# Performance work log

Hardware: AMD Instinct MI355X
Metric: run time of the kernel (lower is better)

## Reference

```python
import jax, jax.numpy as jnp
import numpy as np
from jax import lax

B, C_IN, H, W = 32, 128, 64, 64
K, C_OUT, KS = 8, 128, 3
HID = C_IN * 4  # extend = 4
TEMPERATURE = 1.0
PAD = 1


def setup_inputs() -> dict:
    key = jax.random.key(0)
    ks = jax.random.split(key, 7)
    x = jax.random.normal(ks[0], (B, C_IN, H, W), jnp.float32)
    prompt_param = jax.random.uniform(ks[1], (1, K, HID), jnp.float32)
    w1 = jax.random.normal(ks[2], (HID, C_IN), jnp.float32) * 0.05
    b1 = jnp.zeros((HID,), jnp.float32)
    w2 = jax.random.normal(ks[3], (HID, HID), jnp.float32) * 0.05
    b2 = jnp.zeros((HID,), jnp.float32)
    kernels_weights = jax.random.normal(ks[4], (K, C_OUT, C_IN, KS, KS), jnp.float32) * 0.05
    kernels_bias = jax.random.normal(ks[5], (K, C_OUT), jnp.float32) * 0.05
    return {
        'x': x, 'prompt_param': prompt_param,
        'w1': w1, 'b1': b1, 'w2': w2, 'b2': b2,
        'kernels_weights': kernels_weights, 'kernels_bias': kernels_bias,
    }


def reference(x, prompt_param, w1, b1, w2, b2, kernels_weights, kernels_bias):
    # Attention: global avg pool -> MLP -> prompt dot -> softmax over kernels
    pooled = jnp.mean(x, axis=(2, 3))                       # (B, C_in)
    h = jax.nn.relu(pooled @ w1.T + b1)                     # (B, HID)
    s = h @ w2.T + b2                                       # (B, HID)
    scores = jnp.sum(s[:, None, :] * prompt_param, axis=-1)  # (B, K)
    alphas = jax.nn.softmax(scores / TEMPERATURE, axis=-1)   # (B, K)

    # Per-sample kernel aggregation
    agg_w = jnp.einsum('bk,koihw->boihw', alphas, kernels_weights)  # (B,O,I,kh,kw)
    agg_b = alphas @ kernels_bias                                    # (B, O)

    # Per-sample conv2d (equivalent to the groups=B grouped-conv trick)
    def conv_one(xi, wi):
        # xi: (C_in,H,W), wi: (O,C_in,kh,kw)
        return lax.conv_general_dilated(
            xi[None], wi, window_strides=(1, 1),
            padding=((PAD, PAD), (PAD, PAD)),
            dimension_numbers=('NCHW', 'OIHW', 'NCHW'))[0]
    out = jax.vmap(conv_one)(x, agg_w)                       # (B,O,H,W)
    out = out + agg_b[:, :, None, None]
    return out
```

## Files before the change

kernel.cpp:

```cpp
#include <hip/hip_runtime.h>
#include <hip/hip_bf16.h>
#include <stdint.h>


typedef __bf16 v8bf __attribute__((ext_vector_type(8)));
typedef float  v4f  __attribute__((ext_vector_type(4)));

#define XT_OFF     0u
#define XT_BYTES   (32u*4096u*128u*2u)
#define AGGW_OFF   (XT_OFF + XT_BYTES)
#define AGGW_BYTES (32u*9u*128u*128u*2u)
#define PART_OFF   (AGGW_OFF)
#define POOLED_OFF (AGGW_OFF + 0x100000u)
#define H_OFF      (AGGW_OFF + 0x110000u)
#define PSCORE_OFF (AGGW_OFF + 0x120000u)
#define ALPHA_OFF  (AGGW_OFF + AGGW_BYTES)
#define ALPHA_BYTES (32u*8u*4u)
#define AGGB_OFF   (ALPHA_OFF + ALPHA_BYTES)
#define AGGB_BYTES (32u*128u*4u)

typedef const void __attribute__((address_space(1))) gconst_t;
typedef void       __attribute__((address_space(3))) ldsv_t;

__device__ __forceinline__ void g2l16(const void* g, void* l) {
  __builtin_amdgcn_global_load_lds((gconst_t*)g, (ldsv_t*)l, 16, 0, 0);
}

__global__ __launch_bounds__(256) void pool_convert_kernel(
    const float* __restrict__ x, float* __restrict__ partial,
    __hip_bfloat16* __restrict__ xT) {
  const int b = blockIdx.x >> 6;
  const int h = blockIdx.x & 63;
  const int tid = threadIdx.x;
  const int wv = tid >> 6, lane = tid & 63;
  __shared__ __align__(16) __hip_bfloat16 sT[64 * 130];

  const float* xrow = x + (((size_t)b * 128) << 12) + (h << 6);
  for (int i = 0; i < 32; ++i) {
    int c = wv * 32 + i;
    float v = xrow[((size_t)c << 12) + lane];
    sT[lane * 130 + c] = __float2bfloat16(v);
    float s = v;
    #pragma unroll
    for (int m = 32; m > 0; m >>= 1) s += __shfl_xor(s, m);
    if (lane == 0) partial[((b << 6) + h) * 128 + c] = s;
  }
  __syncthreads();
  const int pw = tid >> 2;
  const int piece = tid & 3;
  const uint32_t* s32 = (const uint32_t*)sT;
  uint32_t vals[16];
  #pragma unroll
  for (int j = 0; j < 16; ++j) vals[j] = s32[pw * 65 + piece * 16 + j];
  char* dst = (char*)xT + ((((size_t)b << 6) + h) * 64 + pw) * 256 + piece * 64;
  #pragma unroll
  for (int j = 0; j < 4; ++j)
    ((uint4*)dst)[j] = make_uint4(vals[4*j], vals[4*j+1], vals[4*j+2], vals[4*j+3]);
}

__global__ __launch_bounds__(128) void pool_reduce_kernel(
    const float* __restrict__ partial, float* __restrict__ pooled) {
  const int b = blockIdx.x, c = threadIdx.x;
  float acc = 0.0f;
  const float* src = partial + ((size_t)b << 6) * 128 + c;
  #pragma unroll 8
  for (int h = 0; h < 64; ++h) acc += src[h * 128];
  pooled[b * 128 + c] = acc * (1.0f / 4096.0f);
}

__global__ __launch_bounds__(256) void attn_l1_kernel(
    const float* __restrict__ pooled, const float* __restrict__ w1,
    const float* __restrict__ b1, float* __restrict__ hbuf) {
  const int jt = blockIdx.x * 8;
  const int tid = threadIdx.x;
  __shared__ float sW[8 * 132];
  __shared__ float sPool[32 * 132];

  {
    int r = tid >> 5, c4 = (tid & 31) * 4;
    *(float4*)&sW[r * 132 + c4] = *(const float4*)&w1[(jt + r) * 128 + c4];
  }
  #pragma unroll
  for (int q = 0; q < 4; ++q) {
    int idx = q * 256 + tid;
    int bb = idx >> 5, c4 = (idx & 31) * 4;
    *(float4*)&sPool[bb * 132 + c4] = *(const float4*)&pooled[bb * 128 + c4];
  }
  __syncthreads();

  const int b = tid >> 3, jr = tid & 7;
  float acc = 0.0f;
  #pragma unroll
  for (int i4 = 0; i4 < 32; ++i4) {
    float4 pv = *(const float4*)&sPool[b * 132 + i4 * 4];
    float4 wv = *(const float4*)&sW[jr * 132 + i4 * 4];
    acc += pv.x * wv.x + pv.y * wv.y + pv.z * wv.z + pv.w * wv.w;
  }
  hbuf[b * 512 + jt + jr] = fmaxf(acc + b1[jt + jr], 0.0f);
}

__global__ __launch_bounds__(256) void attn_l2s_kernel(
    const float* __restrict__ hbuf, const float* __restrict__ w2,
    const float* __restrict__ b2, const float* __restrict__ prompt,
    float* __restrict__ pscore) {
  const int jtile = blockIdx.x >> 1;
  const int bg = blockIdx.x & 1;
  const int jt = jtile * 8;
  const int tid = threadIdx.x;
  __shared__ float sW2[8 * 516];
  __shared__ float sH[16 * 516];
  __shared__ float sSc[16 * 9];
  __shared__ float sPr[64];

  #pragma unroll
  for (int q = 0; q < 4; ++q) {
    int idx = q * 256 + tid;
    int r = idx >> 7, c4 = (idx & 127) * 4;
    *(float4*)&sW2[r * 516 + c4] = *(const float4*)&w2[(jt + r) * 512 + c4];
  }
  #pragma unroll
  for (int q = 0; q < 8; ++q) {
    int idx = q * 256 + tid;
    int r = idx >> 7, c4 = (idx & 127) * 4;
    *(float4*)&sH[r * 516 + c4] =
        *(const float4*)&hbuf[(bg * 16 + r) * 512 + c4];
  }
  if (tid < 64) sPr[tid] = prompt[(tid >> 3) * 512 + jt + (tid & 7)];
  __syncthreads();

  const int pair = tid >> 1, half = tid & 1;
  const int bl = pair >> 3, jr = pair & 7;
  float acc = 0.0f;
  #pragma unroll
  for (int i4 = 0; i4 < 64; ++i4) {
    int idx = (half * 64 + i4) * 4;
    float4 hv = *(const float4*)&sH[bl * 516 + idx];
    float4 wv = *(const float4*)&sW2[jr * 516 + idx];
    acc += hv.x * wv.x + hv.y * wv.y + hv.z * wv.z + hv.w * wv.w;
  }
  acc += __shfl_xor(acc, 1);
  if (half == 0) sSc[bl * 9 + jr] = acc + b2[jt + jr];
  __syncthreads();

  if (tid < 128) {
    int bl = tid >> 3, k = tid & 7;
    float p = 0.0f;
    #pragma unroll
    for (int jj = 0; jj < 8; ++jj) p = fmaf(sSc[bl * 9 + jj], sPr[k * 8 + jj], p);
    pscore[((size_t)(jtile * 32 + bg * 16 + bl)) * 8 + k] = p;
  }
}

__global__ __launch_bounds__(256) void softmax_aggb_kernel(
    const float* __restrict__ pscore, const float* __restrict__ kbias,
    float* __restrict__ alphas, float* __restrict__ aggb) {
  const int b = blockIdx.x;
  const int tid = threadIdx.x;
  __shared__ float sRed[32 * 8], sSc[8], sA[8];

  {
    int jt2 = tid >> 3, k = tid & 7;
    sRed[jt2 * 8 + k] = pscore[((size_t)(jt2 * 32 + b)) * 8 + k] +
                        pscore[((size_t)((jt2 + 32) * 32 + b)) * 8 + k];
  }
  __syncthreads();
  if (tid < 8) {
    float sc = 0.0f;
    #pragma unroll
    for (int j = 0; j < 32; ++j) sc += sRed[j * 8 + tid];
    sSc[tid] = sc;
  }
  __syncthreads();
  if (tid == 0) {
    float mx = sSc[0];
    for (int k = 1; k < 8; ++k) mx = fmaxf(mx, sSc[k]);
    float sum = 0.0f, e[8];
    for (int k = 0; k < 8; ++k) { e[k] = expf(sSc[k] - mx); sum += e[k]; }
    float inv = 1.0f / sum;
    for (int k = 0; k < 8; ++k) sA[k] = e[k] * inv;
  }
  __syncthreads();
  if (tid < 8) alphas[b * 8 + tid] = sA[tid];
  if (tid < 128) {
    float acc = 0.0f;
    #pragma unroll
    for (int k = 0; k < 8; ++k) acc = fmaf(sA[k], kbias[k * 128 + tid], acc);
    aggb[b * 128 + tid] = acc;
  }
}

__global__ __launch_bounds__(128) void agg_weights_kernel(
    const float* __restrict__ kw, const float* __restrict__ alphas,
    __hip_bfloat16* __restrict__ aggw) {
  const int co = blockIdx.x;
  const int bg = blockIdx.y;
  const int tid = threadIdx.x;
  __shared__ float sA[64];
  __shared__ float sbuf[1152];
  if (tid < 64) sA[tid] = alphas[bg * 64 + tid];
  __syncthreads();

  float acc[8][9];
  #pragma unroll
  for (int bb = 0; bb < 8; ++bb)
    #pragma unroll
    for (int q = 0; q < 9; ++q) acc[bb][q] = 0.0f;

  for (int k = 0; k < 8; ++k) {
    const float* src = kw + ((size_t)(k * 128 + co)) * 1152;
    float v[9];
    #pragma unroll
    for (int q = 0; q < 9; ++q) v[q] = src[tid + 128 * q];
    #pragma unroll
    for (int bb = 0; bb < 8; ++bb) {
      float a = sA[bb * 8 + k];
      #pragma unroll
      for (int q = 0; q < 9; ++q) acc[bb][q] = fmaf(a, v[q], acc[bb][q]);
    }
  }

  #pragma unroll 1
  for (int bb = 0; bb < 8; ++bb) {
    __syncthreads();
    #pragma unroll
    for (int q = 0; q < 9; ++q) sbuf[tid + 128 * q] = acc[bb][q];
    __syncthreads();
    const int b = bg * 8 + bb;
    #pragma unroll
    for (int t = 0; t < 9; ++t)
      aggw[(((size_t)(b * 9 + t) * 128 + co) << 7) + tid] =
          __float2bfloat16(sbuf[tid * 9 + t]);
  }
}

#define XTILE_B 33792
#define ATILE_B 8192

__global__ __launch_bounds__(256) void dyn_conv_kernel(
    const __hip_bfloat16* __restrict__ xT, const __hip_bfloat16* __restrict__ aggw,
    const float* __restrict__ aggb, float* __restrict__ out) {
  const int tile = blockIdx.x;
  const int b    = blockIdx.y;
  const int tid  = threadIdx.x;
  const int wv = tid >> 6, lane = tid & 63;
  const int wm = wv >> 1, wn = wv & 1;
  const int lm = lane & 15, quad = lane >> 4;
  const int r0 = tile * 2;

  __shared__ __align__(16) char smem[XTILE_B + 2 * ATILE_B + 512];
  char* xb = smem;
  char* abuf = smem + XTILE_B;
  float* sBias = (float*)(smem + XTILE_B + 2 * ATILE_B);

  if (tid < 128) sBias[tid] = aggb[b * 128 + tid];

  for (int pos = tid; pos < 264; pos += 256) {
    int tr = pos / 66, tc = pos - tr * 66;
    int h = r0 - 1 + tr, w = tc - 1;
    if ((unsigned)h >= 64u || (unsigned)w >= 64u) {
      int4* d = (int4*)(xb + pos * 128);
      #pragma unroll
      for (int i = 0; i < 8; ++i) d[i] = make_int4(0, 0, 0, 0);
    }
  }

  const char* xTb = (const char*)xT + ((size_t)b << 20);
  const char* awb = (const char*)aggw + (size_t)b * 294912;

  auto stageX = [&](int half) {
    for (int i = wv; i < 33; i += 4) {
      int P = (i << 6) + lane;
      int pos = P >> 3, slot = P & 7;
      int tr = pos / 66, tc = pos - tr * 66;
      int h = r0 - 1 + tr, w = tc - 1;
      char* dst = xb + (i << 10);
      if ((unsigned)h < 64u && (unsigned)w < 64u) {
        int p = slot ^ (pos & 7);
        const char* src = xTb + (((h << 6) + w) << 8) + (half << 7) + (p << 4);
        g2l16(src, dst);
      }
    }
  };
  auto stageA = [&](int c) {
    int tap = (c % 18) >> 1;
    int cic = ((c / 18) << 1) | (c & 1);
    char* ab = abuf + (c & 1) * ATILE_B;
    const char* base = awb + (tap << 15);
    #pragma unroll
    for (int jj = 0; jj < 2; ++jj) {
      int j = wv * 2 + jj;
      int co = (j << 4) + (lane >> 2);
      int f = lane & 3;
      int p = f ^ ((co >> 1) & 3);
      const char* src = base + (co << 8) + (cic << 6) + (p << 4);
      g2l16(src, ab + (j << 10));
    }
  };

  int posb[4];
  #pragma unroll
  for (int ni = 0; ni < 4; ++ni) {
    int n = wn * 64 + ni * 16 + lm;
    posb[ni] = (n >> 6) * 66 + (n & 63);
  }
  const int fA = (quad ^ ((lm >> 1) & 3)) << 4;
  int aoff[4];
  #pragma unroll
  for (int mi = 0; mi < 4; ++mi) {
    int co = wm * 64 + mi * 16 + lm;
    aoff[mi] = (co << 6) + fA;
  }

  v4f acc[4][4];
  #pragma unroll
  for (int mi = 0; mi < 4; ++mi)
    #pragma unroll
    for (int ni = 0; ni < 4; ++ni) acc[mi][ni] = v4f{0.f, 0.f, 0.f, 0.f};

  auto computeChunk = [&](int c) {
    int tap = (c % 18) >> 1, sub = c & 1;
    int th = tap / 3, tw = tap - th * 3;
    char* ab = abuf + (c & 1) * ATILE_B;
    v8bf af[4], bfr[4];
    #pragma unroll
    for (int mi = 0; mi < 4; ++mi) af[mi] = *(const v8bf*)(ab + aoff[mi]);
    const int piece = (sub << 2) | quad;
    #pragma unroll
    for (int ni = 0; ni < 4; ++ni) {
      int pos = posb[ni] + th * 66 + tw;
      int pp = (piece ^ (pos & 7)) << 4;
      bfr[ni] = *(const v8bf*)(xb + (pos << 7) + pp);
    }
    #pragma unroll
    for (int mi = 0; mi < 4; ++mi)
      #pragma unroll
      for (int ni = 0; ni < 4; ++ni)
        acc[mi][ni] = __builtin_amdgcn_mfma_f32_16x16x32_bf16(
            af[mi], bfr[ni], acc[mi][ni], 0, 0, 0);
  };

  stageX(0);
  stageA(0);
  __syncthreads();
  for (int c = 0; c < 18; ++c) {
    if (c < 17) stageA(c + 1);
    computeChunk(c);
    __syncthreads();
  }
  stageX(1);
  stageA(18);
  __syncthreads();
  for (int c = 18; c < 36; ++c) {
    if (c < 35) stageA(c + 1);
    computeChunk(c);
    __syncthreads();
  }

  #pragma unroll
  for (int mi = 0; mi < 4; ++mi) {
    #pragma unroll
    for (int r = 0; r < 4; ++r) {
      int co = wm * 64 + mi * 16 + quad * 4 + r;
      float bias = sBias[co];
      #pragma unroll
      for (int ni = 0; ni < 4; ++ni) {
        int n = wn * 64 + ni * 16 + lm;
        out[(((size_t)(b * 128 + co)) << 12) + tile * 128 + n] =
            acc[mi][ni][r] + bias;
      }
    }
  }
}

extern "C" void kernel_launch(void* const* d_in, const int* in_sizes, int n_in,
                              void* d_out, int out_size, void* d_ws, size_t ws_size,
                              hipStream_t stream) {
  const float* x      = (const float*)d_in[0];
  const float* prompt = (const float*)d_in[1];
  const float* w1     = (const float*)d_in[2];
  const float* b1     = (const float*)d_in[3];
  const float* w2     = (const float*)d_in[4];
  const float* b2     = (const float*)d_in[5];
  const float* kw     = (const float*)d_in[6];
  const float* kb     = (const float*)d_in[7];
  float* out = (float*)d_out;
  char* ws = (char*)d_ws;

  __hip_bfloat16* xT   = (__hip_bfloat16*)(ws + XT_OFF);
  __hip_bfloat16* aggw = (__hip_bfloat16*)(ws + AGGW_OFF);
  float* part   = (float*)(ws + PART_OFF);
  float* pooled = (float*)(ws + POOLED_OFF);
  float* hbuf   = (float*)(ws + H_OFF);
  float* pscore = (float*)(ws + PSCORE_OFF);
  float* alphas = (float*)(ws + ALPHA_OFF);
  float* aggb   = (float*)(ws + AGGB_OFF);

  pool_convert_kernel<<<2048, 256, 0, stream>>>(x, part, xT);
  pool_reduce_kernel<<<32, 128, 0, stream>>>(part, pooled);
  attn_l1_kernel<<<64, 256, 0, stream>>>(pooled, w1, b1, hbuf);
  attn_l2s_kernel<<<128, 256, 0, stream>>>(hbuf, w2, b2, prompt, pscore);
  softmax_aggb_kernel<<<32, 256, 0, stream>>>(pscore, kb, alphas, aggb);
  agg_weights_kernel<<<dim3(128, 4), 128, 0, stream>>>(kw, alphas, aggw);
  dyn_conv_kernel<<<dim3(32, 32), 256, 0, stream>>>(xT, aggw, aggb, out);
}
```

Measured before the change: 228.7 us.

## Load conv weights directly from global into registers and quarter-stage input tiles

The dynamic conv kernel no longer stages aggregated weights through LDS. Each wave loads its A fragments straight from global memory with a three-deep register prefetch ring. The input tile is split into four 32-channel quarters, double-buffered in LDS with a new swizzle, which cuts per-chunk barriers from 36 to 3 and shrinks LDS use for higher occupancy. The weight aggregation kernel is also relaunched with one block per (co, batch) and unrolled, trading fewer register accumulators for repeated reads of the kernel weights; the risk is exposed global-load latency for the A fragments.

```diff
diff --git a/kernel.cpp b/kernel.cpp
--- a/kernel.cpp
+++ b/kernel.cpp
@@ -143,11 +143,11 @@
   __syncthreads();
 
   if (tid < 128) {
-    int bl = tid >> 3, k = tid & 7;
+    int bl2 = tid >> 3, k = tid & 7;
     float p = 0.0f;
     #pragma unroll
-    for (int jj = 0; jj < 8; ++jj) p = fmaf(sSc[bl * 9 + jj], sPr[k * 8 + jj], p);
-    pscore[((size_t)(jtile * 32 + bg * 16 + bl)) * 8 + k] = p;
+    for (int jj = 0; jj < 8; ++jj) p = fmaf(sSc[bl2 * 9 + jj], sPr[k * 8 + jj], p);
+    pscore[((size_t)(jtile * 32 + bg * 16 + bl2)) * 8 + k] = p;
   }
 }
 
@@ -193,48 +193,35 @@
     const float* __restrict__ kw, const float* __restrict__ alphas,
     __hip_bfloat16* __restrict__ aggw) {
   const int co = blockIdx.x;
-  const int bg = blockIdx.y;
-  const int tid = threadIdx.x;
-  __shared__ float sA[64];
+  const int b = blockIdx.y;
+  const int ci = threadIdx.x;
+  __shared__ float sA[8];
   __shared__ float sbuf[1152];
-  if (tid < 64) sA[tid] = alphas[bg * 64 + tid];
-  __syncthreads();
-
-  float acc[8][9];
-  #pragma unroll
-  for (int bb = 0; bb < 8; ++bb)
-    #pragma unroll
-    for (int q = 0; q < 9; ++q) acc[bb][q] = 0.0f;
-
+  if (ci < 8) sA[ci] = alphas[b * 8 + ci];
+  __syncthreads();
+
+  float acc[9];
+  #pragma unroll
+  for (int t = 0; t < 9; ++t) acc[t] = 0.0f;
+
+  #pragma unroll
   for (int k = 0; k < 8; ++k) {
-    const float* src = kw + ((size_t)(k * 128 + co)) * 1152;
-    float v[9];
-    #pragma unroll
-    for (int q = 0; q < 9; ++q) v[q] = src[tid + 128 * q];
-    #pragma unroll
-    for (int bb = 0; bb < 8; ++bb) {
-      float a = sA[bb * 8 + k];
-      #pragma unroll
-      for (int q = 0; q < 9; ++q) acc[bb][q] = fmaf(a, v[q], acc[bb][q]);
-    }
-  }
-
-  #pragma unroll 1
-  for (int bb = 0; bb < 8; ++bb) {
-    __syncthreads();
-    #pragma unroll
-    for (int q = 0; q < 9; ++q) sbuf[tid + 128 * q] = acc[bb][q];
-    __syncthreads();
-    const int b = bg * 8 + bb;
-    #pragma unroll
-    for (int t = 0; t < 9; ++t)
-      aggw[(((size_t)(b * 9 + t) * 128 + co) << 7) + tid] =
-          __float2bfloat16(sbuf[tid * 9 + t]);
-  }
-}
-
-#define XTILE_B 33792
-#define ATILE_B 8192
+    const float* src = kw + ((size_t)(k * 128 + co) * 128 + ci) * 9;
+    float a = sA[k];
+    #pragma unroll
+    for (int t = 0; t < 9; ++t) acc[t] = fmaf(a, src[t], acc[t]);
+  }
+
+  #pragma unroll
+  for (int t = 0; t < 9; ++t) sbuf[ci * 9 + t] = acc[t];
+  __syncthreads();
+  #pragma unroll
+  for (int t = 0; t < 9; ++t)
+    aggw[(((size_t)((b * 9 + t) * 128 + co)) << 7) + ci] =
+        __float2bfloat16(sbuf[ci * 9 + t]);
+}
+
+#define XQ_B 16896
 
 __global__ __launch_bounds__(256) void dyn_conv_kernel(
     const __hip_bfloat16* __restrict__ xT, const __hip_bfloat16* __restrict__ aggw,
@@ -247,10 +234,10 @@
   const int lm = lane & 15, quad = lane >> 4;
   const int r0 = tile * 2;
 
-  __shared__ __align__(16) char smem[XTILE_B + 2 * ATILE_B + 512];
-  char* xb = smem;
-  char* abuf = smem + XTILE_B;
-  float* sBias = (float*)(smem + XTILE_B + 2 * ATILE_B);
+  __shared__ __align__(16) char smem[2 * XQ_B + 512];
+  char* xb0 = smem;
+  char* xb1 = smem + XQ_B;
+  float* sBias = (float*)(smem + 2 * XQ_B);
 
   if (tid < 128) sBias[tid] = aggb[b * 128 + tid];
 
@@ -258,44 +245,36 @@
     int tr = pos / 66, tc = pos - tr * 66;
     int h = r0 - 1 + tr, w = tc - 1;
     if ((unsigned)h >= 64u || (unsigned)w >= 64u) {
-      int4* d = (int4*)(xb + pos * 128);
+      int4 z = make_int4(0, 0, 0, 0);
+      int4* d0 = (int4*)(xb0 + (pos << 6));
+      int4* d1 = (int4*)(xb1 + (pos << 6));
       #pragma unroll
-      for (int i = 0; i < 8; ++i) d[i] = make_int4(0, 0, 0, 0);
+      for (int i = 0; i < 4; ++i) { d0[i] = z; d1[i] = z; }
     }
   }
 
   const char* xTb = (const char*)xT + ((size_t)b << 20);
   const char* awb = (const char*)aggw + (size_t)b * 294912;
 
-  auto stageX = [&](int half) {
-    for (int i = wv; i < 33; i += 4) {
+  auto stageX = [&](int q, char* xq) {
+    for (int i = wv; i < 17; i += 4) {
       int P = (i << 6) + lane;
-      int pos = P >> 3, slot = P & 7;
+      int pos = P >> 2, slot = P & 3;
       int tr = pos / 66, tc = pos - tr * 66;
       int h = r0 - 1 + tr, w = tc - 1;
-      char* dst = xb + (i << 10);
-      if ((unsigned)h < 64u && (unsigned)w < 64u) {
-        int p = slot ^ (pos & 7);
-        const char* src = xTb + (((h << 6) + w) << 8) + (half << 7) + (p << 4);
+      char* dst = xq + (i << 10);
+      if (P < 1056 && (unsigned)h < 64u && (unsigned)w < 64u) {
+        int p = slot ^ ((pos >> 1) & 3);
+        const char* src = xTb + (((h << 6) + w) << 8) + (q << 6) + (p << 4);
         g2l16(src, dst);
       }
     }
   };
-  auto stageA = [&](int c) {
-    int tap = (c % 18) >> 1;
-    int cic = ((c / 18) << 1) | (c & 1);
-    char* ab = abuf + (c & 1) * ATILE_B;
-    const char* base = awb + (tap << 15);
-    #pragma unroll
-    for (int jj = 0; jj < 2; ++jj) {
-      int j = wv * 2 + jj;
-      int co = (j << 4) + (lane >> 2);
-      int f = lane & 3;
-      int p = f ^ ((co >> 1) & 3);
-      const char* src = base + (co << 8) + (cic << 6) + (p << 4);
-      g2l16(src, ab + (j << 10));
-    }
-  };
+
+  int aoffB[4];
+  #pragma unroll
+  for (int mi = 0; mi < 4; ++mi)
+    aoffB[mi] = ((wm * 64 + mi * 16 + lm) << 8) + (quad << 4);
 
   int posb[4];
   #pragma unroll
@@ -303,13 +282,6 @@
     int n = wn * 64 + ni * 16 + lm;
     posb[ni] = (n >> 6) * 66 + (n & 63);
   }
-  const int fA = (quad ^ ((lm >> 1) & 3)) << 4;
-  int aoff[4];
-  #pragma unroll
-  for (int mi = 0; mi < 4; ++mi) {
-    int co = wm * 64 + mi * 16 + lm;
-    aoff[mi] = (co << 6) + fA;
-  }
 
   v4f acc[4][4];
   #pragma unroll
@@ -317,43 +289,43 @@
     #pragma unroll
     for (int ni = 0; ni < 4; ++ni) acc[mi][ni] = v4f{0.f, 0.f, 0.f, 0.f};
 
-  auto computeChunk = [&](int c) {
-    int tap = (c % 18) >> 1, sub = c & 1;
+  auto loadA = [&](int tap, int cic, v8bf* dst) {
+    const char* base = awb + (tap << 15) + (cic << 6);
+    #pragma unroll
+    for (int mi = 0; mi < 4; ++mi)
+      dst[mi] = *(const v8bf*)(base + aoffB[mi]);
+  };
+
+  auto computeChunk = [&](int tap, const v8bf* af, const char* xq) {
     int th = tap / 3, tw = tap - th * 3;
-    char* ab = abuf + (c & 1) * ATILE_B;
-    v8bf af[4], bfr[4];
-    #pragma unroll
-    for (int mi = 0; mi < 4; ++mi) af[mi] = *(const v8bf*)(ab + aoff[mi]);
-    const int piece = (sub << 2) | quad;
     #pragma unroll
     for (int ni = 0; ni < 4; ++ni) {
       int pos = posb[ni] + th * 66 + tw;
-      int pp = (piece ^ (pos & 7)) << 4;
-      bfr[ni] = *(const v8bf*)(xb + (pos << 7) + pp);
-    }
-    #pragma unroll
-    for (int mi = 0; mi < 4; ++mi)
+      int sl = (quad ^ ((pos >> 1) & 3)) << 4;
+      v8bf bfr = *(const v8bf*)(xq + (pos << 6) + sl);
       #pragma unroll
-      for (int ni = 0; ni < 4; ++ni)
+      for (int mi = 0; mi < 4; ++mi)
         acc[mi][ni] = __builtin_amdgcn_mfma_f32_16x16x32_bf16(
-            af[mi], bfr[ni], acc[mi][ni], 0, 0, 0);
+            af[mi], bfr, acc[mi][ni], 0, 0, 0);
+    }
   };
 
-  stageX(0);
-  stageA(0);
-  __syncthreads();
-  for (int c = 0; c < 18; ++c) {
-    if (c < 17) stageA(c + 1);
-    computeChunk(c);
-    __syncthreads();
-  }
-  stageX(1);
-  stageA(18);
-  __syncthreads();
-  for (int c = 18; c < 36; ++c) {
-    if (c < 35) stageA(c + 1);
-    computeChunk(c);
-    __syncthreads();
+  v8bf af[3][4];
+  stageX(0, xb0);
+  loadA(0, 0, af[0]);
+  loadA(1, 0, af[1]);
+  __syncthreads();
+  #pragma unroll
+  for (int q = 0; q < 4; ++q) {
+    char* xq = (q & 1) ? xb1 : xb0;
+    if (q < 3) stageX(q + 1, (q & 1) ? xb0 : xb1);
+    #pragma unroll
+    for (int tap = 0; tap < 9; ++tap) {
+      int c = q * 9 + tap;
+      if (c < 34) loadA((c + 2) % 9, (c + 2) / 9, af[(c + 2) % 3]);
+      computeChunk(tap, af[c % 3], xq);
+    }
+    if (q < 3) __syncthreads();
   }
 
   #pragma unroll
@@ -400,6 +372,6 @@
   attn_l1_kernel<<<64, 256, 0, stream>>>(pooled, w1, b1, hbuf);
   attn_l2s_kernel<<<128, 256, 0, stream>>>(hbuf, w2, b2, prompt, pscore);
   softmax_aggb_kernel<<<32, 256, 0, stream>>>(pscore, kb, alphas, aggb);
-  agg_weights_kernel<<<dim3(128, 4), 128, 0, stream>>>(kw, alphas, aggw);
+  agg_weights_kernel<<<dim3(128, 32), 128, 0, stream>>>(kw, alphas, aggw);
   dyn_conv_kernel<<<dim3(32, 32), 256, 0, stream>>>(xT, aggw, aggb, out);
 }
```

Result: slower. 258.8 us (+13.2%).
